# Kernel tuning notes

Hardware: AMD Instinct MI355X
Metric: run time of the kernel (lower is better)

## Reference

```python
import jax, jax.numpy as jnp
import numpy as np


def _side(x, y, W, w):
    # x: [B, Lx, d] attends over y: [B, Ly, d]
    alpha = jnp.einsum('bld,de->ble', x, W)          # bilinear projection
    alpha = jnp.einsum('ble,bme->blm', alpha, y)     # [B, Lx, Ly]
    alpha = jax.nn.softmax(alpha, axis=1)            # Keras softmax axis=1 (over Lx)
    a = jnp.einsum('blm,bmd->bld', alpha, y)         # attended context [B, Lx, d]
    out = jnp.concatenate([x - a, x * a], axis=-1)   # [B, Lx, 2d]
    beta = jax.nn.softmax(jnp.einsum('ble,eo->blo', out, w)[..., 0], axis=-1)  # [B, Lx]
    return jnp.einsum('bl,ble->be', beta, out)       # pooled [B, 2d]


def setup_inputs() -> dict:
    key = jax.random.key(0)
    k1, k2, k3, k4 = jax.random.split(key, 4)
    B, L, d = 512, 256, 512
    return {
        'i': jax.random.normal(k1, (B, L, d), dtype=jnp.float32),
        'j': jax.random.normal(k2, (B, L, d), dtype=jnp.float32),
        'W': jax.random.normal(k3, (d, d), dtype=jnp.float32) * 0.05,
        'w': jax.random.normal(k4, (2 * d, 1), dtype=jnp.float32) * 0.05,
    }


def reference(i, j, W, w):
    out_i = _side(i, j, W, w)
    out_j = _side(j, i, W, w)
    return (out_i, out_j)
```

## Files before the change

### kernel.cpp

```cpp
#include <hip/hip_runtime.h>

#define LL 256
#define DD 512

typedef _Float16 f16;
typedef _Float16 f16x4_t __attribute__((ext_vector_type(4)));
typedef _Float16 f16x8_t __attribute__((ext_vector_type(8)));
typedef float f32x4_t __attribute__((ext_vector_type(4)));

__device__ __forceinline__ f16x8_t cvt2(const float4 a, const float4 b) {
  f16x8_t v;
  v[0] = (f16)a.x; v[1] = (f16)a.y; v[2] = (f16)a.z; v[3] = (f16)a.w;
  v[4] = (f16)b.x; v[5] = (f16)b.y; v[6] = (f16)b.z; v[7] = (f16)b.w;
  return v;
}

__device__ __forceinline__ void gl16(const void* g, void* l) {
  __builtin_amdgcn_global_load_lds(
      (const __attribute__((address_space(1))) void*)g,
      (__attribute__((address_space(3))) void*)l, 16, 0, 0);
}

__global__ void k_prep(const float* __restrict__ W, f16* __restrict__ Wt) {
  __shared__ float t[64][65];
  int bx = blockIdx.x & 7;
  int by = blockIdx.x >> 3;
  int tx = threadIdx.x & 63, tg = threadIdx.x >> 6;
  for (int r = tg; r < 64; r += 4)
    t[r][tx] = W[(by * 64 + r) * DD + bx * 64 + tx];
  __syncthreads();
  for (int r = tg; r < 64; r += 4)
    Wt[(bx * 64 + r) * DD + by * 64 + tx] = (f16)t[tx][r];
}


__global__ __launch_bounds__(512, 2)
void k_main(const float* __restrict__ gi, const float* __restrict__ gj,
            const f16* __restrict__ Wt, const float* __restrict__ wv,
            f16* __restrict__ slabs, float* __restrict__ out) {
  __shared__ __align__(16) char R1[131072];
  __shared__ __align__(16) char R2[16384];

  const int tid = threadIdx.x;
  const int lane = tid & 63;
  const int wave = tid >> 6;
  const int lq = lane & 15, lg = lane >> 4;

  const int sb = blockIdx.x;
  const int wk = (sb & 7) * 128 + (sb >> 3);
  const int b = wk >> 1, side = wk & 1;
  const float* __restrict__ x = (side ? gj : gi) + (size_t)b * (LL * DD);
  const float* __restrict__ y = (side ? gi : gj) + (size_t)b * (LL * DD);
  f16* __restrict__ slab = slabs + (size_t)wk * (LL * DD);

  char* const R1c = R1;
  char* const R2c = R2;
  float* const colred = (float*)R2c;
  float* const colmax = (float*)(R2c + 2048);
  float* const colinv = (float*)(R2c + 3072);
  float* const gp     = (float*)R2c;
  float* const betas  = (float*)(R2c + 2048);

  {
    const int wl2 = wave & 1, we4 = wave >> 1;
    for (int lh = 0; lh < 2; ++lh) {
      f32x4_t acc[4][8];
#pragma unroll
      for (int lf = 0; lf < 4; ++lf)
#pragma unroll
        for (int ef = 0; ef < 8; ++ef) acc[lf][ef] = (f32x4_t){0.f, 0.f, 0.f, 0.f};

      const int xrow = tid >> 2;
      const int xc4 = (tid & 3) * 16;
      {
        const float* src = x + (size_t)(lh * 128 + xrow) * DD + xc4;
        float4 a0 = *(const float4*)src, a1 = *(const float4*)(src + 4);
        float4 a2 = *(const float4*)(src + 8), a3 = *(const float4*)(src + 12);
        unsigned swz = (unsigned)(xrow & 7) << 4;
        *(f16x8_t*)(R1c + xrow * 128 + ((xc4 * 2) ^ swz)) = cvt2(a0, a1);
        *(f16x8_t*)(R1c + xrow * 128 + ((xc4 * 2 + 16) ^ swz)) = cvt2(a2, a3);
      }
      __syncthreads();

      for (int s = 0; s < 8; ++s) {
        char* xbc = R1c + (s & 1) * 16384;
        char* xbn = R1c + ((s + 1) & 1) * 16384;
        float4 p0, p1, p2, p3;
        if (s < 7) {
          const float* src = x + (size_t)(lh * 128 + xrow) * DD + (s + 1) * 64 + xc4;
          p0 = *(const float4*)src; p1 = *(const float4*)(src + 4);
          p2 = *(const float4*)(src + 8); p3 = *(const float4*)(src + 12);
        }
#pragma unroll
        for (int ks = 0; ks < 2; ++ks) {
          f16x8_t aF[4], bF[8];
#pragma unroll
          for (int lf = 0; lf < 4; ++lf) {
            int row = wl2 * 64 + lf * 16 + lq;
            aF[lf] = *(const f16x8_t*)(xbc + row * 128 +
                       ((ks * 64 + lg * 16) ^ ((unsigned)(row & 7) << 4)));
          }
#pragma unroll
          for (int ef = 0; ef < 8; ++ef) {
            int er = we4 * 128 + ef * 16 + lq;
            bF[ef] = *(const f16x8_t*)(Wt + (size_t)er * DD + s * 64 + ks * 32 + lg * 8);
          }
#pragma unroll
          for (int lf = 0; lf < 4; ++lf)
#pragma unroll
            for (int ef = 0; ef < 8; ++ef)
              acc[lf][ef] = __builtin_amdgcn_mfma_f32_16x16x32_f16(aF[lf], bF[ef], acc[lf][ef], 0, 0, 0);
        }
        if (s < 7) {
          unsigned swz = (unsigned)(xrow & 7) << 4;
          *(f16x8_t*)(xbn + xrow * 128 + ((xc4 * 2) ^ swz)) = cvt2(p0, p1);
          *(f16x8_t*)(xbn + xrow * 128 + ((xc4 * 2 + 16) ^ swz)) = cvt2(p2, p3);
        }
        __syncthreads();
      }
#pragma unroll
      for (int lf = 0; lf < 4; ++lf)
#pragma unroll
        for (int ef = 0; ef < 8; ++ef) {
          int e = we4 * 128 + ef * 16 + lq;
          int l0 = lh * 128 + wl2 * 64 + lf * 16 + lg * 4;
#pragma unroll
          for (int r = 0; r < 4; ++r) {
            int l = l0 + r;
            size_t byte = (size_t)l * 1024 + (size_t)(e >> 6) * 128 +
                          (unsigned)(((e & 63) * 2) ^ ((l & 7) << 4));
            *(f16*)((char*)slab + byte) = (f16)acc[lf][ef][r];
          }
        }
    }
  }
  __threadfence_block();
  __syncthreads();

  {
    const int wm = wave & 3, wl = wave >> 2;
    f32x4_t accS[4][8];
#pragma unroll
    for (int mf = 0; mf < 4; ++mf)
#pragma unroll
      for (int nf = 0; nf < 8; ++nf) accS[mf][nf] = (f32x4_t){0.f, 0.f, 0.f, 0.f};

    const int prow = tid >> 1, phalf = tid & 1;
    const int lsub = lane >> 3, lin8 = lane & 7;

    auto stageBP = [&](int s, int buf) {
#pragma unroll
      for (int q = 0; q < 4; ++q) {
        int lrow = (q * 8 + wave) * 8 + lsub;
        const char* g = (const char*)slab + (size_t)lrow * 1024 + (size_t)s * 128 + lin8 * 16;
        gl16(g, R1c + buf * 32768 + (q * 8 + wave) * 1024);
      }
    };

    stageBP(0, 0);
    {
      unsigned swz = (unsigned)(prow & 7) << 4;
      const float* src = y + (size_t)prow * DD + phalf * 32;
#pragma unroll
      for (int q = 0; q < 4; ++q) {
        float4 a0 = *(const float4*)(src + q * 8);
        float4 a1 = *(const float4*)(src + q * 8 + 4);
        *(f16x8_t*)(R1c + 65536 + prow * 128 + ((phalf * 64 + q * 16) ^ swz)) = cvt2(a0, a1);
      }
    }
    __syncthreads();

    for (int s = 0; s < 8; ++s) {
      const char* BPc = R1c + (s & 1) * 32768;
      const char* Yc = R1c + 65536 + (s & 1) * 32768;
      float4 pre_y[8];
      if (s < 7) {
        stageBP(s + 1, (s + 1) & 1);
        const float* src = y + (size_t)prow * DD + (s + 1) * 64 + phalf * 32;
#pragma unroll
        for (int q = 0; q < 8; ++q) pre_y[q] = *(const float4*)(src + q * 4);
      }
#pragma unroll
      for (int ks = 0; ks < 2; ++ks) {
        f16x8_t aF[4], bF[8];
#pragma unroll
        for (int mf = 0; mf < 4; ++mf) {
          int row = wm * 64 + mf * 16 + lq;
          aF[mf] = *(const f16x8_t*)(Yc + row * 128 +
                     ((ks * 64 + lg * 16) ^ ((unsigned)(row & 7) << 4)));
        }
#pragma unroll
        for (int nf = 0; nf < 8; ++nf) {
          int row = wl * 128 + nf * 16 + lq;
          bF[nf] = *(const f16x8_t*)(BPc + row * 128 +
                     ((ks * 64 + lg * 16) ^ ((unsigned)(row & 7) << 4)));
        }
#pragma unroll
        for (int mf = 0; mf < 4; ++mf)
#pragma unroll
          for (int nf = 0; nf < 8; ++nf)
            accS[mf][nf] = __builtin_amdgcn_mfma_f32_16x16x32_f16(aF[mf], bF[nf], accS[mf][nf], 0, 0, 0);
      }
      if (s < 7) {
        char* Yn = R1c + 65536 + ((s + 1) & 1) * 32768;
        unsigned swz = (unsigned)(prow & 7) << 4;
#pragma unroll
        for (int q = 0; q < 4; ++q)
          *(f16x8_t*)(Yn + prow * 128 + ((phalf * 64 + q * 16) ^ swz)) =
              cvt2(pre_y[2 * q], pre_y[2 * q + 1]);
      }
      __syncthreads();
    }

    float red[4][4];
#pragma unroll
    for (int mf = 0; mf < 4; ++mf)
#pragma unroll
      for (int r = 0; r < 4; ++r) {
        float v = accS[mf][0][r];
#pragma unroll
        for (int nf = 1; nf < 8; ++nf) v = fmaxf(v, accS[mf][nf][r]);
        v = fmaxf(v, __shfl_xor(v, 1));
        v = fmaxf(v, __shfl_xor(v, 2));
        v = fmaxf(v, __shfl_xor(v, 4));
        v = fmaxf(v, __shfl_xor(v, 8));
        red[mf][r] = v;
      }
    if (lq == 0) {
#pragma unroll
      for (int mf = 0; mf < 4; ++mf)
#pragma unroll
        for (int r = 0; r < 4; ++r)
          colred[wl * 256 + wm * 64 + mf * 16 + lg * 4 + r] = red[mf][r];
    }
    __syncthreads();
    if (tid < 256) colmax[tid] = fmaxf(colred[tid], colred[256 + tid]);
    __syncthreads();
    float cm[4][4];
#pragma unroll
    for (int mf = 0; mf < 4; ++mf)
#pragma unroll
      for (int r = 0; r < 4; ++r) cm[mf][r] = colmax[wm * 64 + mf * 16 + lg * 4 + r];
    __syncthreads();
#pragma unroll
    for (int mf = 0; mf < 4; ++mf)
#pragma unroll
      for (int r = 0; r < 4; ++r) {
        float s = 0.f;
#pragma unroll
        for (int nf = 0; nf < 8; ++nf) {
          float p = __expf(accS[mf][nf][r] - cm[mf][r]);
          accS[mf][nf][r] = p;
          s += p;
        }
        s += __shfl_xor(s, 1);
        s += __shfl_xor(s, 2);
        s += __shfl_xor(s, 4);
        s += __shfl_xor(s, 8);
        red[mf][r] = s;
      }
    if (lq == 0) {
#pragma unroll
      for (int mf = 0; mf < 4; ++mf)
#pragma unroll
        for (int r = 0; r < 4; ++r)
          colred[wl * 256 + wm * 64 + mf * 16 + lg * 4 + r] = red[mf][r];
    }
    __syncthreads();
    if (tid < 256) colinv[tid] = 1.f / (colred[tid] + colred[256 + tid]);
    __syncthreads();
    float inv[4][4];
#pragma unroll
    for (int mf = 0; mf < 4; ++mf)
#pragma unroll
      for (int r = 0; r < 4; ++r) inv[mf][r] = colinv[wm * 64 + mf * 16 + lg * 4 + r];
    __syncthreads();
#pragma unroll
    for (int mf = 0; mf < 4; ++mf)
#pragma unroll
      for (int nf = 0; nf < 8; ++nf) {
        int l = wl * 128 + nf * 16 + lq;
        f16x4_t v;
        v[0] = (f16)(accS[mf][nf][0] * inv[mf][0]);
        v[1] = (f16)(accS[mf][nf][1] * inv[mf][1]);
        v[2] = (f16)(accS[mf][nf][2] * inv[mf][2]);
        v[3] = (f16)(accS[mf][nf][3] * inv[mf][3]);
        *(f16x4_t*)(R1c + l * 512 +
                    ((wm * 128 + mf * 32 + lg * 8) ^ ((unsigned)(l & 7) << 4))) = v;
      }
  }
  __syncthreads();

  {
    const int wl3 = wave & 3, wd = wave >> 2;
    float garr[4][4];
#pragma unroll
    for (int lf = 0; lf < 4; ++lf)
#pragma unroll
      for (int r = 0; r < 4; ++r) garr[lf][r] = 0.f;

    const int yd = tid & 127, ymq = tid >> 7;
    f16* const a_ = slab;

    for (int dct = 0; dct < 4; ++dct) {
      f32x4_t accB[4][4];
#pragma unroll
      for (int lf = 0; lf < 4; ++lf)
#pragma unroll
        for (int df = 0; df < 4; ++df) accB[lf][df] = (f32x4_t){0.f, 0.f, 0.f, 0.f};

      float lyA[4][4], lyB[4][4];
#pragma unroll
      for (int q = 0; q < 4; ++q) {
        int m0 = ymq * 16 + q * 4;
#pragma unroll
        for (int k = 0; k < 4; ++k)
          lyA[q][k] = y[(size_t)(m0 + k) * DD + dct * 128 + yd];
      }
#pragma unroll
      for (int mh = 0; mh < 4; ++mh) {
        __syncthreads();
        {
          unsigned swz = (unsigned)(yd & 7) << 4;
#pragma unroll
          for (int q = 0; q < 4; ++q) {
            int m0 = ymq * 16 + q * 4;
            f16x4_t v;
            if (mh & 1) {
              v[0] = (f16)lyB[q][0]; v[1] = (f16)lyB[q][1];
              v[2] = (f16)lyB[q][2]; v[3] = (f16)lyB[q][3];
            } else {
              v[0] = (f16)lyA[q][0]; v[1] = (f16)lyA[q][1];
              v[2] = (f16)lyA[q][2]; v[3] = (f16)lyA[q][3];
            }
            *(f16x4_t*)(R2c + yd * 128 + ((m0 * 2) ^ swz)) = v;
          }
        }
        __syncthreads();
        if (mh < 3) {
#pragma unroll
          for (int q = 0; q < 4; ++q) {
            int m0 = (mh + 1) * 64 + ymq * 16 + q * 4;
#pragma unroll
            for (int k = 0; k < 4; ++k) {
              float lv = y[(size_t)(m0 + k) * DD + dct * 128 + yd];
              if (mh & 1) lyA[q][k] = lv; else lyB[q][k] = lv;
            }
          }
        }
#pragma unroll
        for (int ks = 0; ks < 2; ++ks) {
          f16x8_t aF[4], bF[4];
#pragma unroll
          for (int lf = 0; lf < 4; ++lf) {
            int row = wl3 * 64 + lf * 16 + lq;
            aF[lf] = *(const f16x8_t*)(R1c + row * 512 +
                       ((mh * 128 + ks * 64 + lg * 16) ^ ((unsigned)(row & 7) << 4)));
          }
#pragma unroll
          for (int df = 0; df < 4; ++df) {
            int row = wd * 64 + df * 16 + lq;
            bF[df] = *(const f16x8_t*)(R2c + row * 128 +
                       ((ks * 64 + lg * 16) ^ ((unsigned)(row & 7) << 4)));
          }
#pragma unroll
          for (int lf = 0; lf < 4; ++lf)
#pragma unroll
            for (int df = 0; df < 4; ++df)
              accB[lf][df] = __builtin_amdgcn_mfma_f32_16x16x32_f16(aF[lf], bF[df], accB[lf][df], 0, 0, 0);
        }
      }
      float wvA[4], wvB[4];
#pragma unroll
      for (int df = 0; df < 4; ++df) {
        int d = dct * 128 + wd * 64 + df * 16 + lq;
        wvA[df] = wv[d];
        wvB[df] = wv[DD + d];
      }
#pragma unroll
      for (int lf = 0; lf < 4; ++lf)
#pragma unroll
        for (int r = 0; r < 4; ++r) {
          int l = wl3 * 64 + lf * 16 + lg * 4 + r;
          float gs = 0.f;
#pragma unroll
          for (int df = 0; df < 4; ++df) {
            int d = dct * 128 + wd * 64 + df * 16 + lq;
            float av = accB[lf][df][r];
            float xv = x[(size_t)l * DD + d];
            gs += (xv - av) * wvA[df] + (xv * av) * wvB[df];
            a_[(size_t)l * DD + d] = (f16)av;
          }
          gs += __shfl_xor(gs, 1);
          gs += __shfl_xor(gs, 2);
          gs += __shfl_xor(gs, 4);
          gs += __shfl_xor(gs, 8);
          garr[lf][r] += gs;
        }
    }
    __syncthreads();
    if (lq == 0) {
#pragma unroll
      for (int lf = 0; lf < 4; ++lf)
#pragma unroll
        for (int r = 0; r < 4; ++r)
          gp[wd * 256 + wl3 * 64 + lf * 16 + lg * 4 + r] = garr[lf][r];
    }
  }
  __threadfence_block();
  __syncthreads();

  if (wave == 0) {
    float gv[4];
    float M = -3.4e38f;
#pragma unroll
    for (int q = 0; q < 4; ++q) {
      int l = lane + q * 64;
      gv[q] = gp[l] + gp[256 + l];
      M = fmaxf(M, gv[q]);
    }
#pragma unroll
    for (int s = 1; s < 64; s <<= 1) M = fmaxf(M, __shfl_xor(M, s));
    float S = 0.f, ev[4];
#pragma unroll
    for (int q = 0; q < 4; ++q) { ev[q] = __expf(gv[q] - M); S += ev[q]; }
#pragma unroll
    for (int s = 1; s < 64; s <<= 1) S += __shfl_xor(S, s);
    float inv = 1.f / S;
#pragma unroll
    for (int q = 0; q < 4; ++q) betas[lane + q * 64] = ev[q] * inv;
  }
  __syncthreads();

  {
    const f16* const a_ = slab;
    int dc = tid;
    float s1 = 0.f, s2 = 0.f;
    for (int l = 0; l < 256; ++l) {
      float bl = betas[l];
      float av = (float)a_[(size_t)l * DD + dc];
      float xv = x[(size_t)l * DD + dc];
      s1 += bl * (xv - av);
      s2 += bl * (xv * av);
    }
    size_t o = (size_t)side * (512u * 1024u) + (size_t)b * 1024u;
    out[o + dc] = s1;
    out[o + DD + dc] = s2;
  }
}

extern "C" void kernel_launch(void* const* d_in, const int* in_sizes, int n_in,
                              void* d_out, int out_size, void* d_ws, size_t ws_size,
                              hipStream_t stream) {
  (void)in_sizes; (void)n_in; (void)out_size; (void)ws_size;
  const float* gi = (const float*)d_in[0];
  const float* gj = (const float*)d_in[1];
  const float* W  = (const float*)d_in[2];
  const float* wv = (const float*)d_in[3];
  float* out = (float*)d_out;
  f16* Wt = (f16*)d_ws;
  f16* slabs = Wt + DD * DD;
  k_prep<<<dim3(64), dim3(256), 0, stream>>>(W, Wt);
  k_main<<<dim3(1024), dim3(512), 0, stream>>>(gi, gj, Wt, wv, slabs, out);
}
```

Measured before the change: 959.5 us.

## Replace LDS-staged double buffering with direct global fragment loads in all GEMM stages

Drops the shared-memory staging and double buffering of x, y and the projection slab. MFMA operand fragments are now loaded straight from global memory and converted to fp16 in registers. The swizzled slab layout becomes plain row-major, and most block-wide barriers go away. This cuts LDS traffic and synchronisation but costs uncoalesced, redundant global reads, especially the strided per-element y column gathers in the final GEMM, and loses the load/compute overlap.

Measured after the change: 1.129 ms. 17.6% more time.

```diff
diff --git a/kernel.cpp b/kernel.cpp
--- a/kernel.cpp
+++ b/kernel.cpp
@@ -13,12 +13,6 @@
   v[0] = (f16)a.x; v[1] = (f16)a.y; v[2] = (f16)a.z; v[3] = (f16)a.w;
   v[4] = (f16)b.x; v[5] = (f16)b.y; v[6] = (f16)b.z; v[7] = (f16)b.w;
   return v;
-}
-
-__device__ __forceinline__ void gl16(const void* g, void* l) {
-  __builtin_amdgcn_global_load_lds(
-      (const __attribute__((address_space(1))) void*)g,
-      (__attribute__((address_space(3))) void*)l, 16, 0, 0);
 }
 
 __global__ void k_prep(const float* __restrict__ W, f16* __restrict__ Wt) {
@@ -39,7 +33,7 @@
             const f16* __restrict__ Wt, const float* __restrict__ wv,
             f16* __restrict__ slabs, float* __restrict__ out) {
   __shared__ __align__(16) char R1[131072];
-  __shared__ __align__(16) char R2[16384];
+  __shared__ __align__(16) char R2[8192];
 
   const int tid = threadIdx.x;
   const int lane = tid & 63;
@@ -70,53 +64,26 @@
 #pragma unroll
         for (int ef = 0; ef < 8; ++ef) acc[lf][ef] = (f32x4_t){0.f, 0.f, 0.f, 0.f};
 
-      const int xrow = tid >> 2;
-      const int xc4 = (tid & 3) * 16;
-      {
-        const float* src = x + (size_t)(lh * 128 + xrow) * DD + xc4;
-        float4 a0 = *(const float4*)src, a1 = *(const float4*)(src + 4);
-        float4 a2 = *(const float4*)(src + 8), a3 = *(const float4*)(src + 12);
-        unsigned swz = (unsigned)(xrow & 7) << 4;
-        *(f16x8_t*)(R1c + xrow * 128 + ((xc4 * 2) ^ swz)) = cvt2(a0, a1);
-        *(f16x8_t*)(R1c + xrow * 128 + ((xc4 * 2 + 16) ^ swz)) = cvt2(a2, a3);
-      }
-      __syncthreads();
-
-      for (int s = 0; s < 8; ++s) {
-        char* xbc = R1c + (s & 1) * 16384;
-        char* xbn = R1c + ((s + 1) & 1) * 16384;
-        float4 p0, p1, p2, p3;
-        if (s < 7) {
-          const float* src = x + (size_t)(lh * 128 + xrow) * DD + (s + 1) * 64 + xc4;
-          p0 = *(const float4*)src; p1 = *(const float4*)(src + 4);
-          p2 = *(const float4*)(src + 8); p3 = *(const float4*)(src + 12);
-        }
-#pragma unroll
-        for (int ks = 0; ks < 2; ++ks) {
-          f16x8_t aF[4], bF[8];
-#pragma unroll
-          for (int lf = 0; lf < 4; ++lf) {
-            int row = wl2 * 64 + lf * 16 + lq;
-            aF[lf] = *(const f16x8_t*)(xbc + row * 128 +
-                       ((ks * 64 + lg * 16) ^ ((unsigned)(row & 7) << 4)));
-          }
-#pragma unroll
-          for (int ef = 0; ef < 8; ++ef) {
-            int er = we4 * 128 + ef * 16 + lq;
-            bF[ef] = *(const f16x8_t*)(Wt + (size_t)er * DD + s * 64 + ks * 32 + lg * 8);
-          }
-#pragma unroll
-          for (int lf = 0; lf < 4; ++lf)
-#pragma unroll
-            for (int ef = 0; ef < 8; ++ef)
-              acc[lf][ef] = __builtin_amdgcn_mfma_f32_16x16x32_f16(aF[lf], bF[ef], acc[lf][ef], 0, 0, 0);
-        }
-        if (s < 7) {
-          unsigned swz = (unsigned)(xrow & 7) << 4;
-          *(f16x8_t*)(xbn + xrow * 128 + ((xc4 * 2) ^ swz)) = cvt2(p0, p1);
-          *(f16x8_t*)(xbn + xrow * 128 + ((xc4 * 2 + 16) ^ swz)) = cvt2(p2, p3);
-        }
-        __syncthreads();
+#pragma unroll 2
+      for (int s = 0; s < 16; ++s) {
+        f16x8_t aF[4], bF[8];
+#pragma unroll
+        for (int lf = 0; lf < 4; ++lf) {
+          int l = lh * 128 + wl2 * 64 + lf * 16 + lq;
+          const float* src = x + (size_t)l * DD + s * 32 + lg * 8;
+          float4 a0 = *(const float4*)src, a1 = *(const float4*)(src + 4);
+          aF[lf] = cvt2(a0, a1);
+        }
+#pragma unroll
+        for (int ef = 0; ef < 8; ++ef) {
+          int e = we4 * 128 + ef * 16 + lq;
+          bF[ef] = *(const f16x8_t*)(Wt + (size_t)e * DD + s * 32 + lg * 8);
+        }
+#pragma unroll
+        for (int lf = 0; lf < 4; ++lf)
+#pragma unroll
+          for (int ef = 0; ef < 8; ++ef)
+            acc[lf][ef] = __builtin_amdgcn_mfma_f32_16x16x32_f16(aF[lf], bF[ef], acc[lf][ef], 0, 0, 0);
       }
 #pragma unroll
       for (int lf = 0; lf < 4; ++lf)
@@ -125,12 +92,8 @@
           int e = we4 * 128 + ef * 16 + lq;
           int l0 = lh * 128 + wl2 * 64 + lf * 16 + lg * 4;
 #pragma unroll
-          for (int r = 0; r < 4; ++r) {
-            int l = l0 + r;
-            size_t byte = (size_t)l * 1024 + (size_t)(e >> 6) * 128 +
-                          (unsigned)(((e & 63) * 2) ^ ((l & 7) << 4));
-            *(f16*)((char*)slab + byte) = (f16)acc[lf][ef][r];
-          }
+          for (int r = 0; r < 4; ++r)
+            slab[(size_t)(l0 + r) * DD + e] = (f16)acc[lf][ef][r];
         }
     }
   }
@@ -145,55 +108,22 @@
 #pragma unroll
       for (int nf = 0; nf < 8; ++nf) accS[mf][nf] = (f32x4_t){0.f, 0.f, 0.f, 0.f};
 
-    const int prow = tid >> 1, phalf = tid & 1;
-    const int lsub = lane >> 3, lin8 = lane & 7;
-
-    auto stageBP = [&](int s, int buf) {
-#pragma unroll
-      for (int q = 0; q < 4; ++q) {
-        int lrow = (q * 8 + wave) * 8 + lsub;
-        const char* g = (const char*)slab + (size_t)lrow * 1024 + (size_t)s * 128 + lin8 * 16;
-        gl16(g, R1c + buf * 32768 + (q * 8 + wave) * 1024);
-      }
-    };
-
-    stageBP(0, 0);
-    {
-      unsigned swz = (unsigned)(prow & 7) << 4;
-      const float* src = y + (size_t)prow * DD + phalf * 32;
-#pragma unroll
-      for (int q = 0; q < 4; ++q) {
-        float4 a0 = *(const float4*)(src + q * 8);
-        float4 a1 = *(const float4*)(src + q * 8 + 4);
-        *(f16x8_t*)(R1c + 65536 + prow * 128 + ((phalf * 64 + q * 16) ^ swz)) = cvt2(a0, a1);
-      }
-    }
-    __syncthreads();
-
+#pragma unroll 2
     for (int s = 0; s < 8; ++s) {
-      const char* BPc = R1c + (s & 1) * 32768;
-      const char* Yc = R1c + 65536 + (s & 1) * 32768;
-      float4 pre_y[8];
-      if (s < 7) {
-        stageBP(s + 1, (s + 1) & 1);
-        const float* src = y + (size_t)prow * DD + (s + 1) * 64 + phalf * 32;
-#pragma unroll
-        for (int q = 0; q < 8; ++q) pre_y[q] = *(const float4*)(src + q * 4);
-      }
 #pragma unroll
       for (int ks = 0; ks < 2; ++ks) {
         f16x8_t aF[4], bF[8];
 #pragma unroll
         for (int mf = 0; mf < 4; ++mf) {
-          int row = wm * 64 + mf * 16 + lq;
-          aF[mf] = *(const f16x8_t*)(Yc + row * 128 +
-                     ((ks * 64 + lg * 16) ^ ((unsigned)(row & 7) << 4)));
+          int m = wm * 64 + mf * 16 + lq;
+          const float* src = y + (size_t)m * DD + s * 64 + ks * 32 + lg * 8;
+          float4 a0 = *(const float4*)src, a1 = *(const float4*)(src + 4);
+          aF[mf] = cvt2(a0, a1);
         }
 #pragma unroll
         for (int nf = 0; nf < 8; ++nf) {
-          int row = wl * 128 + nf * 16 + lq;
-          bF[nf] = *(const f16x8_t*)(BPc + row * 128 +
-                     ((ks * 64 + lg * 16) ^ ((unsigned)(row & 7) << 4)));
+          int l = wl * 128 + nf * 16 + lq;
+          bF[nf] = *(const f16x8_t*)(slab + (size_t)l * DD + s * 64 + ks * 32 + lg * 8);
         }
 #pragma unroll
         for (int mf = 0; mf < 4; ++mf)
@@ -201,15 +131,6 @@
           for (int nf = 0; nf < 8; ++nf)
             accS[mf][nf] = __builtin_amdgcn_mfma_f32_16x16x32_f16(aF[mf], bF[nf], accS[mf][nf], 0, 0, 0);
       }
-      if (s < 7) {
-        char* Yn = R1c + 65536 + ((s + 1) & 1) * 32768;
-        unsigned swz = (unsigned)(prow & 7) << 4;
-#pragma unroll
-        for (int q = 0; q < 4; ++q)
-          *(f16x8_t*)(Yn + prow * 128 + ((phalf * 64 + q * 16) ^ swz)) =
-              cvt2(pre_y[2 * q], pre_y[2 * q + 1]);
-      }
-      __syncthreads();
     }
 
     float red[4][4];
@@ -274,7 +195,6 @@
     for (int mf = 0; mf < 4; ++mf)
 #pragma unroll
       for (int r = 0; r < 4; ++r) inv[mf][r] = colinv[wm * 64 + mf * 16 + lg * 4 + r];
-    __syncthreads();
 #pragma unroll
     for (int mf = 0; mf < 4; ++mf)
 #pragma unroll
@@ -299,7 +219,6 @@
 #pragma unroll
       for (int r = 0; r < 4; ++r) garr[lf][r] = 0.f;
 
-    const int yd = tid & 127, ymq = tid >> 7;
     f16* const a_ = slab;
 
     for (int dct = 0; dct < 4; ++dct) {
@@ -309,67 +228,31 @@
 #pragma unroll
         for (int df = 0; df < 4; ++df) accB[lf][df] = (f32x4_t){0.f, 0.f, 0.f, 0.f};
 
-      float lyA[4][4], lyB[4][4];
-#pragma unroll
-      for (int q = 0; q < 4; ++q) {
-        int m0 = ymq * 16 + q * 4;
-#pragma unroll
-        for (int k = 0; k < 4; ++k)
-          lyA[q][k] = y[(size_t)(m0 + k) * DD + dct * 128 + yd];
-      }
-#pragma unroll
-      for (int mh = 0; mh < 4; ++mh) {
-        __syncthreads();
-        {
-          unsigned swz = (unsigned)(yd & 7) << 4;
-#pragma unroll
-          for (int q = 0; q < 4; ++q) {
-            int m0 = ymq * 16 + q * 4;
-            f16x4_t v;
-            if (mh & 1) {
-              v[0] = (f16)lyB[q][0]; v[1] = (f16)lyB[q][1];
-              v[2] = (f16)lyB[q][2]; v[3] = (f16)lyB[q][3];
-            } else {
-              v[0] = (f16)lyA[q][0]; v[1] = (f16)lyA[q][1];
-              v[2] = (f16)lyA[q][2]; v[3] = (f16)lyA[q][3];
-            }
-            *(f16x4_t*)(R2c + yd * 128 + ((m0 * 2) ^ swz)) = v;
-          }
-        }
-        __syncthreads();
-        if (mh < 3) {
-#pragma unroll
-          for (int q = 0; q < 4; ++q) {
-            int m0 = (mh + 1) * 64 + ymq * 16 + q * 4;
-#pragma unroll
-            for (int k = 0; k < 4; ++k) {
-              float lv = y[(size_t)(m0 + k) * DD + dct * 128 + yd];
-              if (mh & 1) lyA[q][k] = lv; else lyB[q][k] = lv;
-            }
-          }
-        }
-#pragma unroll
-        for (int ks = 0; ks < 2; ++ks) {
-          f16x8_t aF[4], bF[4];
-#pragma unroll
-          for (int lf = 0; lf < 4; ++lf) {
-            int row = wl3 * 64 + lf * 16 + lq;
-            aF[lf] = *(const f16x8_t*)(R1c + row * 512 +
-                       ((mh * 128 + ks * 64 + lg * 16) ^ ((unsigned)(row & 7) << 4)));
-          }
-#pragma unroll
-          for (int df = 0; df < 4; ++df) {
-            int row = wd * 64 + df * 16 + lq;
-            bF[df] = *(const f16x8_t*)(R2c + row * 128 +
-                       ((ks * 64 + lg * 16) ^ ((unsigned)(row & 7) << 4)));
-          }
-#pragma unroll
-          for (int lf = 0; lf < 4; ++lf)
-#pragma unroll
-            for (int df = 0; df < 4; ++df)
-              accB[lf][df] = __builtin_amdgcn_mfma_f32_16x16x32_f16(aF[lf], bF[df], accB[lf][df], 0, 0, 0);
-        }
-      }
+#pragma unroll 2
+      for (int ms = 0; ms < 8; ++ms) {
+        f16x8_t aF[4], bF[4];
+#pragma unroll
+        for (int lf = 0; lf < 4; ++lf) {
+          int row = wl3 * 64 + lf * 16 + lq;
+          aF[lf] = *(const f16x8_t*)(R1c + row * 512 +
+                     ((ms * 64 + lg * 16) ^ ((unsigned)(row & 7) << 4)));
+        }
+#pragma unroll
+        for (int df = 0; df < 4; ++df) {
+          int d = dct * 128 + wd * 64 + df * 16 + lq;
+          const float* src = y + (size_t)(ms * 32 + lg * 8) * DD + d;
+          f16x8_t v;
+#pragma unroll
+          for (int j = 0; j < 8; ++j) v[j] = (f16)src[(size_t)j * DD];
+          bF[df] = v;
+        }
+#pragma unroll
+        for (int lf = 0; lf < 4; ++lf)
+#pragma unroll
+          for (int df = 0; df < 4; ++df)
+            accB[lf][df] = __builtin_amdgcn_mfma_f32_16x16x32_f16(aF[lf], bF[df], accB[lf][df], 0, 0, 0);
+      }
+
       float wvA[4], wvB[4];
 #pragma unroll
       for (int df = 0; df < 4; ++df) {
@@ -398,6 +281,7 @@
           garr[lf][r] += gs;
         }
     }
+    __threadfence_block();
     __syncthreads();
     if (lq == 0) {
 #pragma unroll
@@ -407,7 +291,6 @@
           gp[wd * 256 + wl3 * 64 + lf * 16 + lg * 4 + r] = garr[lf][r];
     }
   }
-  __threadfence_block();
   __syncthreads();
 
   if (wave == 0) {
```
